# Kernel tuning notes

Hardware: AMD Instinct MI355X
Metric: run time of the kernel (lower is better)

Reference implementation:

```python
import jax, jax.numpy as jnp
import numpy as np

B, S, U, M = 4096, 64, 128, 32
ODE_UNFOLDS = 6
EPS = 1e-08

def _uniform(k, shape, lo, hi):
    return jax.random.uniform(k, shape, jnp.float32, lo, hi)

def setup_inputs() -> dict:
    key = jax.random.key(0)
    ks = jax.random.split(key, 16)
    return {
        "inputs": jax.random.normal(ks[0], (B, S), jnp.float32),
        "state": jax.random.normal(ks[1], (B, U), jnp.float32),
        "gleak": _uniform(ks[2], (U,), 0.001, 1.0),
        "vleak": _uniform(ks[3], (U,), -0.2, 0.2),
        "cm": _uniform(ks[4], (U,), 0.4, 0.6),
        "sigma": _uniform(ks[5], (U, U), 3.0, 8.0),
        "mu": _uniform(ks[6], (U, U), 0.3, 0.8),
        "w": _uniform(ks[7], (U, U), 0.001, 1.0),
        "erev": jnp.sign(jax.random.normal(ks[8], (U, U), jnp.float32)),
        "sensory_sigma": _uniform(ks[9], (S, U), 3.0, 8.0),
        "sensory_mu": _uniform(ks[10], (S, U), 0.3, 0.8),
        "sensory_w": _uniform(ks[11], (S, U), 0.001, 1.0),
        "sensory_erev": jnp.sign(jax.random.normal(ks[12], (S, U), jnp.float32)),
        "sparsity_mask": (jax.random.uniform(ks[13], (U, U)) < 0.5).astype(jnp.float32),
        "sensory_sparsity_mask": (jax.random.uniform(ks[14], (S, U)) < 0.5).astype(jnp.float32),
        "input_w": jnp.ones((S,), jnp.float32),
        "input_b": jnp.zeros((S,), jnp.float32),
        "output_w": jnp.ones((M,), jnp.float32),
        "output_b": jnp.zeros((M,), jnp.float32),
    }

def reference(inputs, state, gleak, vleak, cm, sigma, mu, w, erev,
              sensory_sigma, sensory_mu, sensory_w, sensory_erev,
              sparsity_mask, sensory_sparsity_mask,
              input_w, input_b, output_w, output_b):
    # input mapping (affine)
    x = inputs * input_w + input_b                       # [B,S]
    # sensory synapse activation: [B,S,U]
    sens_act = (sensory_w * sensory_sparsity_mask) * jax.nn.sigmoid(
        sensory_sigma * (x[:, :, None] - sensory_mu))
    w_num_sensory = jnp.sum(sens_act * sensory_erev, axis=1)   # [B,U]
    w_den_sensory = jnp.sum(sens_act, axis=1)                  # [B,U]

    wm = w * sparsity_mask                                     # masked weights [U,U]
    wme = wm * erev                                            # weights*erev   [U,U]
    cm_t = cm * ODE_UNFOLDS                                    # cm / (1/unfolds)
    leak = gleak * vleak

    v = state
    for _ in range(ODE_UNFOLDS):
        sig = jax.nn.sigmoid(sigma * (v[:, :, None] - mu))     # [B,U,U] (src,dst)
        w_num = jnp.einsum('bsu,su->bu', sig, wme) + w_num_sensory
        w_den = jnp.einsum('bsu,su->bu', sig, wm) + w_den_sensory
        v = (cm_t * v + leak + w_num) / (cm_t + gleak + w_den + EPS)

    out = v[:, :M] * output_w + output_b                       # motor slice + affine
    return out, v
```

## Files before the change

kernel.cpp:

```cpp
#include <hip/hip_runtime.h>
#include <hip/hip_fp16.h>

typedef unsigned short u16;
typedef unsigned int   u32;

#define B_TOTAL 4096
#define NU      128
#define NS      64
#define NM      32
#define UNFOLDS 6
#define LOG2E   1.44269504088896340736f

__device__ __forceinline__ float bf2f(u16 v) {
  return __uint_as_float(((u32)v) << 16);
}
__device__ __forceinline__ u16 f2bf(float f) {
  u32 x = __float_as_uint(f);
  return (u16)((x + 0x7fffu + ((x >> 16) & 1u)) >> 16);
}

template<bool BF16>
__device__ __forceinline__ float LD(const void* p, int i) {
  if (BF16) return bf2f(((const u16*)p)[i]);
  return ((const float*)p)[i];
}

__device__ __forceinline__ u32 pk(float a, float b) {
  __half2 h = __halves2half2(__float2half_rn(a), __float2half_rn(b));
  return __builtin_bit_cast(u32, h);
}
__device__ __forceinline__ float lo2f(u32 h) {
  return __low2float(__builtin_bit_cast(__half2, h));
}
__device__ __forceinline__ float hi2f(u32 h) {
  return __high2float(__builtin_bit_cast(__half2, h));
}

__device__ __forceinline__ void step2i(uint4 a, float va, float vb,
                                       float& na0, float& da0, float& na1, float& da1,
                                       float& nb0, float& db0, float& nb1, float& db1) {
  float ta0 = fmaf(va, lo2f(a.x), lo2f(a.y));
  float ta1 = fmaf(va, hi2f(a.x), hi2f(a.y));
  float tb0 = fmaf(vb, lo2f(a.x), lo2f(a.y));
  float tb1 = fmaf(vb, hi2f(a.x), hi2f(a.y));
  float ea0 = __builtin_amdgcn_exp2f(ta0);
  float ea1 = __builtin_amdgcn_exp2f(ta1);
  float eb0 = __builtin_amdgcn_exp2f(tb0);
  float eb1 = __builtin_amdgcn_exp2f(tb1);
  float pa0 = 1.0f + ea0, pa1 = 1.0f + ea1;
  float pb0 = 1.0f + eb0, pb1 = 1.0f + eb1;
  float ra = __builtin_amdgcn_rcpf(pa0 * pa1);
  float rb = __builtin_amdgcn_rcpf(pb0 * pb1);
  float sa0 = pa1 * ra, sa1 = pa0 * ra;
  float sb0 = pb1 * rb, sb1 = pb0 * rb;
  na0 = fmaf(sa0, lo2f(a.z), na0);  da0 = fmaf(sa0, lo2f(a.w), da0);
  na1 = fmaf(sa1, hi2f(a.z), na1);  da1 = fmaf(sa1, hi2f(a.w), da1);
  nb0 = fmaf(sb0, lo2f(a.z), nb0);  db0 = fmaf(sb0, lo2f(a.w), db0);
  nb1 = fmaf(sb1, hi2f(a.z), nb1);  db1 = fmaf(sb1, hi2f(a.w), db1);
}

template<bool BF16>
__device__ __forceinline__ void body(
    const void* g_in, const void* g_state, const void* g_gleak, const void* g_vleak,
    const void* g_cm, const void* g_sigma, const void* g_mu, const void* g_w,
    const void* g_erev, const void* g_ssig, const void* g_smu, const void* g_sw,
    const void* g_serev, const void* g_mask, const void* g_smask,
    const void* g_iw, const void* g_ib, const void* g_ow, const void* g_ob,
    void* g_out,
    uint4* smR,
    float* smV,
    float* smP)
{
  const int tid = threadIdx.x;
  const int b0  = blockIdx.x * 16;

  const int wv  = tid >> 6;
  const int u0  = tid & 63;
  const int u1  = u0 + 64;
  const int p   = wv & 7;
  const bool hiW = wv >= 8;
  const int ba = b0 + 2 * p;
  const int bb = ba + 1;

  float* vbA = smV + p * 256;
  float* vbB = vbA + 128;
  float* red = smP + p * 512;

  #pragma unroll 4
  for (int e = tid; e < NS * 64; e += 1024) {
    int s = e >> 6, l = e & 63;
    int i0 = s * NU + l, i1 = i0 + 64;
    float sl0 = LD<BF16>(g_ssig, i0) * LOG2E, sl1 = LD<BF16>(g_ssig, i1) * LOG2E;
    float ms0 = LD<BF16>(g_smu, i0) * sl0,    ms1 = LD<BF16>(g_smu, i1) * sl1;
    float w0 = LD<BF16>(g_sw, i0) * LD<BF16>(g_smask, i0) * LD<BF16>(g_serev, i0);
    float w1 = LD<BF16>(g_sw, i1) * LD<BF16>(g_smask, i1) * LD<BF16>(g_serev, i1);
    smR[e] = make_uint4(pk(-sl0, -sl1), pk(ms0, ms1), pk(w0, w1),
                        pk(fabsf(w0), fabsf(w1)));
  }

  float va0 = 0.f, va1 = 0.f, vb0 = 0.f, vb1 = 0.f;
  if (!hiW) {
    float iw = LD<BF16>(g_iw, u0), ib = LD<BF16>(g_ib, u0);
    float xa = LD<BF16>(g_in, ba * NS + u0) * iw + ib;
    float xb = LD<BF16>(g_in, bb * NS + u0) * iw + ib;
    va0 = LD<BF16>(g_state, ba * NU + u0);
    va1 = LD<BF16>(g_state, ba * NU + u1);
    vb0 = LD<BF16>(g_state, bb * NU + u0);
    vb1 = LD<BF16>(g_state, bb * NU + u1);
    vbA[u0] = xa;
    vbB[u0] = xb;
  }
  const float gl0 = LD<BF16>(g_gleak, u0), gl1 = LD<BF16>(g_gleak, u1);
  const float lk0 = gl0 * LD<BF16>(g_vleak, u0);
  const float lk1 = gl1 * LD<BF16>(g_vleak, u1);
  const float cm0 = LD<BF16>(g_cm, u0) * (float)UNFOLDS;
  const float cm1 = LD<BF16>(g_cm, u1) * (float)UNFOLDS;
  const float cgl0 = cm0 + gl0 + 1e-8f;
  const float cgl1 = cm1 + gl1 + 1e-8f;

  const uint4* pR = smR + u0;
  const int sbase = hiW ? 32 : 0;
  const int jbase = hiW ? 64 : 0;

  __syncthreads();

  float nsa0 = 0.f, dsa0 = 0.f, nsa1 = 0.f, dsa1 = 0.f;
  float nsb0 = 0.f, dsb0 = 0.f, nsb1 = 0.f, dsb1 = 0.f;
  #pragma unroll 4
  for (int s4 = 0; s4 < 32; s4 += 4) {
    float4 xa4 = *(const float4*)(vbA + sbase + s4);
    float4 xb4 = *(const float4*)(vbB + sbase + s4);
    step2i(pR[(sbase + s4 + 0) * 64], xa4.x, xb4.x, nsa0, dsa0, nsa1, dsa1, nsb0, dsb0, nsb1, dsb1);
    step2i(pR[(sbase + s4 + 1) * 64], xa4.y, xb4.y, nsa0, dsa0, nsa1, dsa1, nsb0, dsb0, nsb1, dsb1);
    step2i(pR[(sbase + s4 + 2) * 64], xa4.z, xb4.z, nsa0, dsa0, nsa1, dsa1, nsb0, dsb0, nsb1, dsb1);
    step2i(pR[(sbase + s4 + 3) * 64], xa4.w, xb4.w, nsa0, dsa0, nsa1, dsa1, nsb0, dsb0, nsb1, dsb1);
  }
  __syncthreads();

  if (!hiW) {
    vbA[u0] = va0;  vbA[u1] = va1;
    vbB[u0] = vb0;  vbB[u1] = vb1;
  }

  #pragma unroll 4
  for (int e = tid; e < NU * 64; e += 1024) {
    int j = e >> 6, l = e & 63;
    int i0 = j * NU + l, i1 = i0 + 64;
    float sl0 = LD<BF16>(g_sigma, i0) * LOG2E, sl1 = LD<BF16>(g_sigma, i1) * LOG2E;
    float ms0 = LD<BF16>(g_mu, i0) * sl0,      ms1 = LD<BF16>(g_mu, i1) * sl1;
    float w0 = LD<BF16>(g_w, i0) * LD<BF16>(g_mask, i0) * LD<BF16>(g_erev, i0);
    float w1 = LD<BF16>(g_w, i1) * LD<BF16>(g_mask, i1) * LD<BF16>(g_erev, i1);
    smR[e] = make_uint4(pk(-sl0, -sl1), pk(ms0, ms1), pk(w0, w1),
                        pk(fabsf(w0), fabsf(w1)));
  }
  __syncthreads();

  #pragma unroll 1
  for (int it = 0; it < UNFOLDS; ++it) {
    float na0 = nsa0, da0 = dsa0, na1 = nsa1, da1 = dsa1;
    float nb0 = nsb0, db0 = dsb0, nb1 = nsb1, db1 = dsb1;
    #pragma unroll 4
    for (int j4 = 0; j4 < 64; j4 += 4) {
      float4 va4 = *(const float4*)(vbA + jbase + j4);
      float4 vb4 = *(const float4*)(vbB + jbase + j4);
      step2i(pR[(jbase + j4 + 0) * 64], va4.x, vb4.x, na0, da0, na1, da1, nb0, db0, nb1, db1);
      step2i(pR[(jbase + j4 + 1) * 64], va4.y, vb4.y, na0, da0, na1, da1, nb0, db0, nb1, db1);
      step2i(pR[(jbase + j4 + 2) * 64], va4.z, vb4.z, na0, da0, na1, da1, nb0, db0, nb1, db1);
      step2i(pR[(jbase + j4 + 3) * 64], va4.w, vb4.w, na0, da0, na1, da1, nb0, db0, nb1, db1);
    }
    if (hiW) {
      red[0 * 64 + u0] = na0;  red[1 * 64 + u0] = da0;
      red[2 * 64 + u0] = na1;  red[3 * 64 + u0] = da1;
      red[4 * 64 + u0] = nb0;  red[5 * 64 + u0] = db0;
      red[6 * 64 + u0] = nb1;  red[7 * 64 + u0] = db1;
    }
    __syncthreads();
    if (!hiW) {
      na0 += red[0 * 64 + u0];  da0 += red[1 * 64 + u0];
      na1 += red[2 * 64 + u0];  da1 += red[3 * 64 + u0];
      nb0 += red[4 * 64 + u0];  db0 += red[5 * 64 + u0];
      nb1 += red[6 * 64 + u0];  db1 += red[7 * 64 + u0];
      va0 = fmaf(cm0, va0, lk0 + na0) * __builtin_amdgcn_rcpf(cgl0 + da0);
      va1 = fmaf(cm1, va1, lk1 + na1) * __builtin_amdgcn_rcpf(cgl1 + da1);
      vb0 = fmaf(cm0, vb0, lk0 + nb0) * __builtin_amdgcn_rcpf(cgl0 + db0);
      vb1 = fmaf(cm1, vb1, lk1 + nb1) * __builtin_amdgcn_rcpf(cgl1 + db1);
      if (it < UNFOLDS - 1) {
        vbA[u0] = va0;  vbA[u1] = va1;
        vbB[u0] = vb0;  vbB[u1] = vb1;
      }
    }
    __syncthreads();
  }

  if (!hiW) {
    if (BF16) {
      u16* om = (u16*)g_out;
      u16* ov = om + B_TOTAL * NM;
      ov[ba * NU + u0] = f2bf(va0);
      ov[ba * NU + u1] = f2bf(va1);
      ov[bb * NU + u0] = f2bf(vb0);
      ov[bb * NU + u1] = f2bf(vb1);
      if (u0 < NM) {
        float ow = LD<true>(g_ow, u0), ob = LD<true>(g_ob, u0);
        om[ba * NM + u0] = f2bf(fmaf(va0, ow, ob));
        om[bb * NM + u0] = f2bf(fmaf(vb0, ow, ob));
      }
    } else {
      float* om = (float*)g_out;
      float* ov = om + B_TOTAL * NM;
      ov[ba * NU + u0] = va0;
      ov[ba * NU + u1] = va1;
      ov[bb * NU + u0] = vb0;
      ov[bb * NU + u1] = vb1;
      if (u0 < NM) {
        float ow = LD<false>(g_ow, u0), ob = LD<false>(g_ob, u0);
        om[ba * NM + u0] = fmaf(va0, ow, ob);
        om[bb * NM + u0] = fmaf(vb0, ow, ob);
      }
    }
  }
}

__global__ __launch_bounds__(1024, 4) void ltc_kernel(
    const void* g_in, const void* g_state, const void* g_gleak, const void* g_vleak,
    const void* g_cm, const void* g_sigma, const void* g_mu, const void* g_w,
    const void* g_erev, const void* g_ssig, const void* g_smu, const void* g_sw,
    const void* g_serev, const void* g_mask, const void* g_smask,
    const void* g_iw, const void* g_ib, const void* g_ow, const void* g_ob,
    void* g_out)
{
  __shared__ uint4 smR[NU * 64];
  __shared__ float smV[8 * 256];
  __shared__ float smP[8 * 512];

  const u16* sg = (const u16*)g_sigma;
  int cnt = 0;
  #pragma unroll
  for (int i = 0; i < 32; ++i) {
    float f = bf2f(sg[2 * i]);
    cnt += (f >= 2.0f && f <= 16.0f) ? 1 : 0;
  }
  if (cnt >= 24)
    body<true >(g_in, g_state, g_gleak, g_vleak, g_cm, g_sigma, g_mu, g_w, g_erev,
                g_ssig, g_smu, g_sw, g_serev, g_mask, g_smask,
                g_iw, g_ib, g_ow, g_ob, g_out, smR, smV, smP);
  else
    body<false>(g_in, g_state, g_gleak, g_vleak, g_cm, g_sigma, g_mu, g_w, g_erev,
                g_ssig, g_smu, g_sw, g_serev, g_mask, g_smask,
                g_iw, g_ib, g_ow, g_ob, g_out, smR, smV, smP);
}

extern "C" void kernel_launch(void* const* d_in, const int* in_sizes, int n_in,
                              void* d_out, int out_size, void* d_ws, size_t ws_size,
                              hipStream_t stream) {
  (void)in_sizes; (void)n_in; (void)out_size; (void)d_ws; (void)ws_size;
  dim3 grid(B_TOTAL / 16);
  dim3 block(1024);
  hipLaunchKernelGGL(ltc_kernel, grid, block, 0, stream,
                     d_in[0], d_in[1], d_in[2], d_in[3], d_in[4],
                     d_in[5], d_in[6], d_in[7], d_in[8],
                     d_in[9], d_in[10], d_in[11], d_in[12],
                     d_in[13], d_in[14], d_in[15], d_in[16],
                     d_in[17], d_in[18], d_out);
}
```

Measured before the change: 193.6 us.

## Use fma_mix for fp16 operands and split reduction/update across wave halves

Replaces separate half-to-float conversions plus fmaf with v_fma_mix_f32 inline asm that reads the packed fp16 operands directly, so fewer VALU instructions are issued in the inner sigmoid loop. It also changes the cross-wave reduction so each half of the waves owns one batch row: each writes the partial sums the other half needs, then reduces and updates its own row. The per-iteration serial update tail is shared by both wave halves instead of running on half of them while the other half idles. Inline asm may limit compiler scheduling.

```diff
diff --git a/kernel.cpp b/kernel.cpp
--- a/kernel.cpp
+++ b/kernel.cpp
@@ -29,20 +29,35 @@
   __half2 h = __halves2half2(__float2half_rn(a), __float2half_rn(b));
   return __builtin_bit_cast(u32, h);
 }
-__device__ __forceinline__ float lo2f(u32 h) {
-  return __low2float(__builtin_bit_cast(__half2, h));
-}
-__device__ __forceinline__ float hi2f(u32 h) {
-  return __high2float(__builtin_bit_cast(__half2, h));
-}
-
-__device__ __forceinline__ void step2i(uint4 a, float va, float vb,
+
+__device__ __forceinline__ float mixfma_ll(float a, u32 b, u32 c) {
+  float d;
+  asm("v_fma_mix_f32 %0, %1, %2, %3 op_sel:[0,0,0] op_sel_hi:[0,1,1]"
+      : "=v"(d) : "v"(a), "v"(b), "v"(c));
+  return d;
+}
+__device__ __forceinline__ float mixfma_hh(float a, u32 b, u32 c) {
+  float d;
+  asm("v_fma_mix_f32 %0, %1, %2, %3 op_sel:[0,1,1] op_sel_hi:[0,1,1]"
+      : "=v"(d) : "v"(a), "v"(b), "v"(c));
+  return d;
+}
+__device__ __forceinline__ void mixacc_lo(float& acc, float s, u32 w) {
+  asm("v_fma_mix_f32 %0, %1, %2, %0 op_sel:[0,0,0] op_sel_hi:[0,1,0]"
+      : "+v"(acc) : "v"(s), "v"(w));
+}
+__device__ __forceinline__ void mixacc_hi(float& acc, float s, u32 w) {
+  asm("v_fma_mix_f32 %0, %1, %2, %0 op_sel:[0,1,0] op_sel_hi:[0,1,0]"
+      : "+v"(acc) : "v"(s), "v"(w));
+}
+
+__device__ __forceinline__ void step2m(uint4 a, float va, float vb,
                                        float& na0, float& da0, float& na1, float& da1,
                                        float& nb0, float& db0, float& nb1, float& db1) {
-  float ta0 = fmaf(va, lo2f(a.x), lo2f(a.y));
-  float ta1 = fmaf(va, hi2f(a.x), hi2f(a.y));
-  float tb0 = fmaf(vb, lo2f(a.x), lo2f(a.y));
-  float tb1 = fmaf(vb, hi2f(a.x), hi2f(a.y));
+  float ta0 = mixfma_ll(va, a.x, a.y);
+  float ta1 = mixfma_hh(va, a.x, a.y);
+  float tb0 = mixfma_ll(vb, a.x, a.y);
+  float tb1 = mixfma_hh(vb, a.x, a.y);
   float ea0 = __builtin_amdgcn_exp2f(ta0);
   float ea1 = __builtin_amdgcn_exp2f(ta1);
   float eb0 = __builtin_amdgcn_exp2f(tb0);
@@ -53,10 +68,10 @@
   float rb = __builtin_amdgcn_rcpf(pb0 * pb1);
   float sa0 = pa1 * ra, sa1 = pa0 * ra;
   float sb0 = pb1 * rb, sb1 = pb0 * rb;
-  na0 = fmaf(sa0, lo2f(a.z), na0);  da0 = fmaf(sa0, lo2f(a.w), da0);
-  na1 = fmaf(sa1, hi2f(a.z), na1);  da1 = fmaf(sa1, hi2f(a.w), da1);
-  nb0 = fmaf(sb0, lo2f(a.z), nb0);  db0 = fmaf(sb0, lo2f(a.w), db0);
-  nb1 = fmaf(sb1, hi2f(a.z), nb1);  db1 = fmaf(sb1, hi2f(a.w), db1);
+  mixacc_lo(na0, sa0, a.z);  mixacc_lo(da0, sa0, a.w);
+  mixacc_hi(na1, sa1, a.z);  mixacc_hi(da1, sa1, a.w);
+  mixacc_lo(nb0, sb0, a.z);  mixacc_lo(db0, sb0, a.w);
+  mixacc_hi(nb1, sb1, a.z);  mixacc_hi(db1, sb1, a.w);
 }
 
 template<bool BF16>
@@ -81,9 +96,11 @@
   const bool hiW = wv >= 8;
   const int ba = b0 + 2 * p;
   const int bb = ba + 1;
+  const int rown = hiW ? bb : ba;
 
   float* vbA = smV + p * 256;
   float* vbB = vbA + 128;
+  float* myStrip = hiW ? vbB : vbA;
   float* red = smP + p * 512;
 
   #pragma unroll 4
@@ -98,18 +115,13 @@
                         pk(fabsf(w0), fabsf(w1)));
   }
 
-  float va0 = 0.f, va1 = 0.f, vb0 = 0.f, vb1 = 0.f;
-  if (!hiW) {
+  {
     float iw = LD<BF16>(g_iw, u0), ib = LD<BF16>(g_ib, u0);
-    float xa = LD<BF16>(g_in, ba * NS + u0) * iw + ib;
-    float xb = LD<BF16>(g_in, bb * NS + u0) * iw + ib;
-    va0 = LD<BF16>(g_state, ba * NU + u0);
-    va1 = LD<BF16>(g_state, ba * NU + u1);
-    vb0 = LD<BF16>(g_state, bb * NU + u0);
-    vb1 = LD<BF16>(g_state, bb * NU + u1);
-    vbA[u0] = xa;
-    vbB[u0] = xb;
-  }
+    float x = LD<BF16>(g_in, rown * NS + u0) * iw + ib;
+    myStrip[u0] = x;
+  }
+  float v0 = LD<BF16>(g_state, rown * NU + u0);
+  float v1 = LD<BF16>(g_state, rown * NU + u1);
   const float gl0 = LD<BF16>(g_gleak, u0), gl1 = LD<BF16>(g_gleak, u1);
   const float lk0 = gl0 * LD<BF16>(g_vleak, u0);
   const float lk1 = gl1 * LD<BF16>(g_vleak, u1);
@@ -130,17 +142,14 @@
   for (int s4 = 0; s4 < 32; s4 += 4) {
     float4 xa4 = *(const float4*)(vbA + sbase + s4);
     float4 xb4 = *(const float4*)(vbB + sbase + s4);
-    step2i(pR[(sbase + s4 + 0) * 64], xa4.x, xb4.x, nsa0, dsa0, nsa1, dsa1, nsb0, dsb0, nsb1, dsb1);
-    step2i(pR[(sbase + s4 + 1) * 64], xa4.y, xb4.y, nsa0, dsa0, nsa1, dsa1, nsb0, dsb0, nsb1, dsb1);
-    step2i(pR[(sbase + s4 + 2) * 64], xa4.z, xb4.z, nsa0, dsa0, nsa1, dsa1, nsb0, dsb0, nsb1, dsb1);
-    step2i(pR[(sbase + s4 + 3) * 64], xa4.w, xb4.w, nsa0, dsa0, nsa1, dsa1, nsb0, dsb0, nsb1, dsb1);
+    step2m(pR[(sbase + s4 + 0) * 64], xa4.x, xb4.x, nsa0, dsa0, nsa1, dsa1, nsb0, dsb0, nsb1, dsb1);
+    step2m(pR[(sbase + s4 + 1) * 64], xa4.y, xb4.y, nsa0, dsa0, nsa1, dsa1, nsb0, dsb0, nsb1, dsb1);
+    step2m(pR[(sbase + s4 + 2) * 64], xa4.z, xb4.z, nsa0, dsa0, nsa1, dsa1, nsb0, dsb0, nsb1, dsb1);
+    step2m(pR[(sbase + s4 + 3) * 64], xa4.w, xb4.w, nsa0, dsa0, nsa1, dsa1, nsb0, dsb0, nsb1, dsb1);
   }
   __syncthreads();
 
-  if (!hiW) {
-    vbA[u0] = va0;  vbA[u1] = va1;
-    vbB[u0] = vb0;  vbB[u1] = vb1;
-  }
+  myStrip[u0] = v0;  myStrip[u1] = v1;
 
   #pragma unroll 4
   for (int e = tid; e < NU * 64; e += 1024) {
@@ -163,60 +172,52 @@
     for (int j4 = 0; j4 < 64; j4 += 4) {
       float4 va4 = *(const float4*)(vbA + jbase + j4);
       float4 vb4 = *(const float4*)(vbB + jbase + j4);
-      step2i(pR[(jbase + j4 + 0) * 64], va4.x, vb4.x, na0, da0, na1, da1, nb0, db0, nb1, db1);
-      step2i(pR[(jbase + j4 + 1) * 64], va4.y, vb4.y, na0, da0, na1, da1, nb0, db0, nb1, db1);
-      step2i(pR[(jbase + j4 + 2) * 64], va4.z, vb4.z, na0, da0, na1, da1, nb0, db0, nb1, db1);
-      step2i(pR[(jbase + j4 + 3) * 64], va4.w, vb4.w, na0, da0, na1, da1, nb0, db0, nb1, db1);
+      step2m(pR[(jbase + j4 + 0) * 64], va4.x, vb4.x, na0, da0, na1, da1, nb0, db0, nb1, db1);
+      step2m(pR[(jbase + j4 + 1) * 64], va4.y, vb4.y, na0, da0, na1, da1, nb0, db0, nb1, db1);
+      step2m(pR[(jbase + j4 + 2) * 64], va4.z, vb4.z, na0, da0, na1, da1, nb0, db0, nb1, db1);
+      step2m(pR[(jbase + j4 + 3) * 64], va4.w, vb4.w, na0, da0, na1, da1, nb0, db0, nb1, db1);
     }
     if (hiW) {
       red[0 * 64 + u0] = na0;  red[1 * 64 + u0] = da0;
       red[2 * 64 + u0] = na1;  red[3 * 64 + u0] = da1;
+    } else {
       red[4 * 64 + u0] = nb0;  red[5 * 64 + u0] = db0;
       red[6 * 64 + u0] = nb1;  red[7 * 64 + u0] = db1;
     }
     __syncthreads();
-    if (!hiW) {
-      na0 += red[0 * 64 + u0];  da0 += red[1 * 64 + u0];
-      na1 += red[2 * 64 + u0];  da1 += red[3 * 64 + u0];
-      nb0 += red[4 * 64 + u0];  db0 += red[5 * 64 + u0];
-      nb1 += red[6 * 64 + u0];  db1 += red[7 * 64 + u0];
-      va0 = fmaf(cm0, va0, lk0 + na0) * __builtin_amdgcn_rcpf(cgl0 + da0);
-      va1 = fmaf(cm1, va1, lk1 + na1) * __builtin_amdgcn_rcpf(cgl1 + da1);
-      vb0 = fmaf(cm0, vb0, lk0 + nb0) * __builtin_amdgcn_rcpf(cgl0 + db0);
-      vb1 = fmaf(cm1, vb1, lk1 + nb1) * __builtin_amdgcn_rcpf(cgl1 + db1);
-      if (it < UNFOLDS - 1) {
-        vbA[u0] = va0;  vbA[u1] = va1;
-        vbB[u0] = vb0;  vbB[u1] = vb1;
-      }
+    float n0, d0, n1, d1;
+    if (hiW) {
+      n0 = nb0 + red[4 * 64 + u0];  d0 = db0 + red[5 * 64 + u0];
+      n1 = nb1 + red[6 * 64 + u0];  d1 = db1 + red[7 * 64 + u0];
+    } else {
+      n0 = na0 + red[0 * 64 + u0];  d0 = da0 + red[1 * 64 + u0];
+      n1 = na1 + red[2 * 64 + u0];  d1 = da1 + red[3 * 64 + u0];
+    }
+    v0 = fmaf(cm0, v0, lk0 + n0) * __builtin_amdgcn_rcpf(cgl0 + d0);
+    v1 = fmaf(cm1, v1, lk1 + n1) * __builtin_amdgcn_rcpf(cgl1 + d1);
+    if (it < UNFOLDS - 1) {
+      myStrip[u0] = v0;  myStrip[u1] = v1;
     }
     __syncthreads();
   }
 
-  if (!hiW) {
-    if (BF16) {
-      u16* om = (u16*)g_out;
-      u16* ov = om + B_TOTAL * NM;
-      ov[ba * NU + u0] = f2bf(va0);
-      ov[ba * NU + u1] = f2bf(va1);
-      ov[bb * NU + u0] = f2bf(vb0);
-      ov[bb * NU + u1] = f2bf(vb1);
-      if (u0 < NM) {
-        float ow = LD<true>(g_ow, u0), ob = LD<true>(g_ob, u0);
-        om[ba * NM + u0] = f2bf(fmaf(va0, ow, ob));
-        om[bb * NM + u0] = f2bf(fmaf(vb0, ow, ob));
-      }
-    } else {
-      float* om = (float*)g_out;
-      float* ov = om + B_TOTAL * NM;
-      ov[ba * NU + u0] = va0;
-      ov[ba * NU + u1] = va1;
-      ov[bb * NU + u0] = vb0;
-      ov[bb * NU + u1] = vb1;
-      if (u0 < NM) {
-        float ow = LD<false>(g_ow, u0), ob = LD<false>(g_ob, u0);
-        om[ba * NM + u0] = fmaf(va0, ow, ob);
-        om[bb * NM + u0] = fmaf(vb0, ow, ob);
-      }
+  if (BF16) {
+    u16* om = (u16*)g_out;
+    u16* ov = om + B_TOTAL * NM;
+    ov[rown * NU + u0] = f2bf(v0);
+    ov[rown * NU + u1] = f2bf(v1);
+    if (u0 < NM) {
+      float ow = LD<true>(g_ow, u0), ob = LD<true>(g_ob, u0);
+      om[rown * NM + u0] = f2bf(fmaf(v0, ow, ob));
+    }
+  } else {
+    float* om = (float*)g_out;
+    float* ov = om + B_TOTAL * NM;
+    ov[rown * NU + u0] = v0;
+    ov[rown * NU + u1] = v1;
+    if (u0 < NM) {
+      float ow = LD<false>(g_ow, u0), ob = LD<false>(g_ob, u0);
+      om[rown * NM + u0] = fmaf(v0, ow, ob);
     }
   }
 }
```

Result: slower. 204.9 us (+5.9%).
